# Optimization experiments

Measured on AMD Instinct MI355X. Metric: run time of the kernel, lower is better.

## Reference

```python
import jax, jax.numpy as jnp
import numpy as np

B, C, H, W = 4, 64, 96, 96
KS, NH = 7, 4


def setup_inputs() -> dict:
    key = jax.random.key(0)
    ks = jax.random.split(key, 9)
    s = 0.1  # keep logits in a sane range for softmax
    return {
        "input_x": jax.random.normal(ks[0], (B, C, H, W), jnp.float32),
        "q_w": jax.random.normal(ks[1], (C, C), jnp.float32) * s,
        "q_b": jax.random.normal(ks[2], (C,), jnp.float32) * s,
        "k_w": jax.random.normal(ks[3], (C, C), jnp.float32) * s,
        "k_b": jax.random.normal(ks[4], (C,), jnp.float32) * s,
        "v_w": jax.random.normal(ks[5], (C, C), jnp.float32) * s,
        "v_b": jax.random.normal(ks[6], (C,), jnp.float32) * s,
        "rel_h": jax.random.normal(ks[7], (C // 2, KS, 1), jnp.float32) * s,
        "rel_w": jax.random.normal(ks[8], (C // 2, 1, KS), jnp.float32) * s,
    }


def _unfold(x, ks):
    # x: (B, C, Hp, Wp) -> (B, C, Ho, Wo, ks, ks), same as torch .unfold(2).unfold(3)
    Hp, Wp = x.shape[2], x.shape[3]
    Ho, Wo = Hp - ks + 1, Wp - ks + 1
    ih = jnp.arange(Ho)[:, None] + jnp.arange(ks)[None, :]  # (Ho, ks)
    iw = jnp.arange(Wo)[:, None] + jnp.arange(ks)[None, :]  # (Wo, ks)
    return x[:, :, ih[:, None, :, None], iw[None, :, None, :]]


def reference(input_x, q_w, q_b, k_w, k_b, v_w, v_b, rel_h, rel_w):
    b, c, h, w = input_x.shape
    ks, nh = KS, NH
    dkh = c // nh
    p0 = (ks - 1) // 2
    p1 = ks - 1 - p0
    padded = jnp.pad(input_x, ((0, 0), (0, 0), (p0, p1), (p0, p1)))

    conv1x1 = lambda x, wt, bi: jnp.einsum('bchw,oc->bohw', x, wt) + bi[None, :, None, None]
    k = conv1x1(padded, k_w, k_b)
    v = conv1x1(padded, v_w, v_b)
    q = conv1x1(input_x, q_w, q_b)

    # flat reshapes exactly as in torch (row-major), reproducing its layout semantics
    k = _unfold(k, ks).reshape(b, nh, h, w, dkh, ks * ks)
    v = _unfold(v, ks).reshape(b, nh, h, w, dkh, ks * ks)
    q = q.reshape(b, nh, h, w, dkh)  # torch: (b,nh,h,w,dkh,1) squeezed

    qk = jnp.einsum('bnxyd,bnxydk->bnxyk', q, k).reshape(b, nh, h, w, ks, ks)
    # torch einsum 'bhxydz,cij->bhxyij' == (sum_d q) outer (sum_c rel)
    qsum = q.sum(-1)  # (b, nh, h, w)
    rel = rel_h.sum(0) + rel_w.sum(0)  # broadcasts to (ks, ks)
    qk = qk + qsum[..., None, None] * rel

    weights = jax.nn.softmax(qk.reshape(b, nh, h, w, ks * ks), axis=-1)
    attn = jnp.einsum('bnxyk,bnxydk->bnxyd', weights, v)  # (b, nh, h, w, dkh)
    attn = attn.reshape(b, c, h, w)  # flat reshape, matching torch
    return jax.nn.relu(attn)
```

## Files before the change

### kernel.cpp

```cpp
#include <hip/hip_runtime.h>

#define B_ 4
#define C_ 64
#define H_ 96
#define W_ 96
#define KS_ 7
#define NPIX (H_ * W_)
#define LDSTR 108

typedef __attribute__((ext_vector_type(8))) short short8;
typedef __attribute__((ext_vector_type(4))) float f32x4;

static __device__ inline ushort f2bf(float f) {
    union { float f; unsigned u; } v; v.f = f;
    unsigned r = (v.u + 0x7fff + ((v.u >> 16) & 1)) >> 16;
    return (ushort)r;
}


__global__ __launch_bounds__(256) void mfma_conv_kernel(
    const float* __restrict__ in,
    const float* __restrict__ qw, const float* __restrict__ qb,
    const float* __restrict__ kw, const float* __restrict__ kb,
    const float* __restrict__ vw, const float* __restrict__ vb,
    float* __restrict__ qkv)
{
    const int b    = blockIdx.y;
    const int pix0 = blockIdx.x * 32;
    const int t    = threadIdx.x;
    const int lane = t & 63;
    const int wv   = t >> 6;

    __shared__ ushort wlds[192 * 64];
    __shared__ ushort xs[32 * 64];
    __shared__ float  bias_s[192];

    #pragma unroll
    for (int g = 0; g < 12; ++g) {
        const int qq  = t + 256 * g;
        const int row = qq >> 4;
        const int c4  = (qq & 15) * 4;
        const float* src = (row < 64) ? qw + row * 64
                         : (row < 128) ? kw + (row - 64) * 64
                                       : vw + (row - 128) * 64;
        float4 f = *reinterpret_cast<const float4*>(src + c4);
        ushort4 u = make_ushort4(f2bf(f.x), f2bf(f.y), f2bf(f.z), f2bf(f.w));
        unsigned byte = (unsigned)(row * 128 + c4 * 2) ^ (unsigned)((row & 7) << 4);
        *reinterpret_cast<ushort4*>(reinterpret_cast<char*>(wlds) + byte) = u;
    }
    if (t < 192) {
        const int tensor = t >> 6;
        bias_s[t] = (tensor == 0 ? qb : tensor == 1 ? kb : vb)[t & 63];
    }
    {
        const int pix = t & 31, cg = t >> 5;
        const float* xp = in + (size_t)b * C_ * NPIX + pix0 + pix;
        #pragma unroll
        for (int g = 0; g < 2; ++g) {
            const int ch = (cg + 8 * g) * 4;
            float x0 = xp[(size_t)(ch    ) * NPIX];
            float x1 = xp[(size_t)(ch + 1) * NPIX];
            float x2 = xp[(size_t)(ch + 2) * NPIX];
            float x3 = xp[(size_t)(ch + 3) * NPIX];
            ushort4 u = make_ushort4(f2bf(x0), f2bf(x1), f2bf(x2), f2bf(x3));
            unsigned byte = (unsigned)(pix * 128 + ch * 2) ^ (unsigned)((pix & 7) << 4);
            *reinterpret_cast<ushort4*>(reinterpret_cast<char*>(xs) + byte) = u;
        }
    }
    __syncthreads();

    short8 afr[3][2];
    #pragma unroll
    for (int i = 0; i < 3; ++i) {
        const int row = (3 * wv + i) * 16 + (lane & 15);
        #pragma unroll
        for (int ka = 0; ka < 2; ++ka) {
            const int kk = ka * 32 + (lane >> 4) * 8;
            unsigned byte = (unsigned)(row * 128 + kk * 2) ^ (unsigned)((row & 7) << 4);
            afr[i][ka] = *reinterpret_cast<const short8*>(
                reinterpret_cast<const char*>(wlds) + byte);
        }
    }
    short8 bfr[2][2];
    #pragma unroll
    for (int nt = 0; nt < 2; ++nt) {
        const int pl = nt * 16 + (lane & 15);
        #pragma unroll
        for (int ka = 0; ka < 2; ++ka) {
            const int kk = ka * 32 + (lane >> 4) * 8;
            unsigned byte = (unsigned)(pl * 128 + kk * 2) ^ (unsigned)((pl & 7) << 4);
            bfr[nt][ka] = *reinterpret_cast<const short8*>(
                reinterpret_cast<const char*>(xs) + byte);
        }
    }
    f32x4 acc[3][2];
    #pragma unroll
    for (int i = 0; i < 3; ++i) {
        f32x4 bi;
        #pragma unroll
        for (int r = 0; r < 4; ++r)
            bi[r] = bias_s[(3 * wv + i) * 16 + (lane >> 4) * 4 + r];
        #pragma unroll
        for (int nt = 0; nt < 2; ++nt) acc[i][nt] = bi;
    }
    #pragma unroll
    for (int i = 0; i < 3; ++i) {
        #pragma unroll
        for (int nt = 0; nt < 2; ++nt) {
            acc[i][nt] = __builtin_amdgcn_mfma_f32_16x16x32_bf16(
                afr[i][0], bfr[nt][0], acc[i][nt], 0, 0, 0);
            acc[i][nt] = __builtin_amdgcn_mfma_f32_16x16x32_bf16(
                afr[i][1], bfr[nt][1], acc[i][nt], 0, 0, 0);
        }
    }
    #pragma unroll
    for (int i = 0; i < 3; ++i) {
        #pragma unroll
        for (int r = 0; r < 4; ++r) {
            const int row = (3 * wv + i) * 16 + (lane >> 4) * 4 + r;
            float* op = qkv + ((size_t)b * 192 + row) * NPIX + pix0 + (lane & 15);
            #pragma unroll
            for (int nt = 0; nt < 2; ++nt)
                op[nt * 16] = acc[i][nt][r];
        }
    }
}

__global__ __launch_bounds__(384) void attn_kernel(
    const float* __restrict__ qkv,
    const float* __restrict__ kb, const float* __restrict__ vb,
    const float* __restrict__ relh, const float* __restrict__ relw,
    float* __restrict__ out)
{
    const int bx   = blockIdx.x;
    const int tile = bx % 3;
    const int c    = (bx / 3) % C_;
    const int b    = bx / (3 * C_);
    const int ho0  = tile * 32;
    const int t    = threadIdx.x;

    __shared__ float ks[38 * LDSTR];
    __shared__ float vs[38 * LDSTR];
    __shared__ float rel_s[49];

    if (t < 49) {
        const int i = t / KS_, j = t % KS_;
        float s = 0.f;
        #pragma unroll
        for (int cc = 0; cc < C_ / 2; ++cc)
            s += relh[cc * KS_ + i] + relw[cc * KS_ + j];
        rel_s[t] = s;
    }
    {
        const float kbias = kb[c];
        const float vbias = vb[c];
        const float* kg = qkv + ((size_t)b * 192 +  64 + c) * NPIX;
        const float* vg = qkv + ((size_t)b * 192 + 128 + c) * NPIX;
        for (int idx = t; idx < 38 * 104; idx += 384) {
            const int rl = idx / 104, cl = idx - rl * 104;
            const int gr = ho0 + rl - 3, gc = cl - 3;
            const bool inb = (gr >= 0 && gr < H_ && gc >= 0 && gc < W_);
            const int gi = gr * W_ + gc;
            ks[rl * LDSTR + cl] = inb ? kg[gi] : kbias;
            vs[rl * LDSTR + cl] = inb ? vg[gi] : vbias;
        }
    }
    __syncthreads();

    const int r0   = t / 12;
    const int rest = t % 12;
    const int w0   = (rest >> 1) * 16;
    const int half = rest & 1;
    const int ho   = ho0 + r0;

    const float* qp = qkv + ((size_t)b * 192 + c) * NPIX + ho * W_ + w0;
    float qs[16];
    #pragma unroll
    for (int tt = 0; tt < 16; tt += 4) {
        float4 f = *reinterpret_cast<const float4*>(qp + tt);
        qs[tt] = f.x; qs[tt + 1] = f.y; qs[tt + 2] = f.z; qs[tt + 3] = f.w;
    }
    float qsum = 0.f;
    #pragma unroll
    for (int tt = 0; tt < 16; ++tt) qsum += qs[tt];

    float logit[49];
    #pragma unroll
    for (int i = 0; i < KS_; ++i) {
        float kr[22];
        const float* kp = &ks[(r0 + i) * LDSTR + w0];
        #pragma unroll
        for (int tt = 0; tt < 20; tt += 4) {
            float4 f = *reinterpret_cast<const float4*>(kp + tt);
            kr[tt] = f.x; kr[tt + 1] = f.y; kr[tt + 2] = f.z; kr[tt + 3] = f.w;
        }
        float2 f2 = *reinterpret_cast<const float2*>(kp + 20);
        kr[20] = f2.x; kr[21] = f2.y;
        #pragma unroll
        for (int j = 0; j < KS_; ++j) {
            float s0 = 0.f, s1 = 0.f, s2 = 0.f, s3 = 0.f;
            #pragma unroll
            for (int tt = 0; tt < 16; tt += 4) {
                s0 = fmaf(qs[tt],     kr[tt + j],     s0);
                s1 = fmaf(qs[tt + 1], kr[tt + 1 + j], s1);
                s2 = fmaf(qs[tt + 2], kr[tt + 2 + j], s2);
                s3 = fmaf(qs[tt + 3], kr[tt + 3 + j], s3);
            }
            logit[i * KS_ + j] = (s0 + s1) + (s2 + s3) + qsum * rel_s[i * KS_ + j];
        }
    }

    float m0 = logit[0], m1 = logit[1], m2 = logit[2], m3 = logit[3];
    #pragma unroll
    for (int kk = 4; kk < 48; kk += 4) {
        m0 = fmaxf(m0, logit[kk]);
        m1 = fmaxf(m1, logit[kk + 1]);
        m2 = fmaxf(m2, logit[kk + 2]);
        m3 = fmaxf(m3, logit[kk + 3]);
    }
    float m = fmaxf(fmaxf(m0, m1), fmaxf(m2, m3));
    m = fmaxf(m, logit[48]);

    float e0 = 0.f, e1 = 0.f, e2 = 0.f, e3 = 0.f;
    #pragma unroll
    for (int kk = 0; kk < 48; kk += 4) {
        float a0 = __expf(logit[kk]     - m);
        float a1 = __expf(logit[kk + 1] - m);
        float a2 = __expf(logit[kk + 2] - m);
        float a3 = __expf(logit[kk + 3] - m);
        logit[kk] = a0; logit[kk + 1] = a1; logit[kk + 2] = a2; logit[kk + 3] = a3;
        e0 += a0; e1 += a1; e2 += a2; e3 += a3;
    }
    float a48 = __expf(logit[48] - m);
    logit[48] = a48;
    const float inv = 1.f / ((e0 + e1) + (e2 + e3) + a48);

    float o8[8];
    #pragma unroll
    for (int d = 0; d < 8; ++d) o8[d] = 0.f;

    #pragma unroll
    for (int i = 0; i < KS_; ++i) {
        float vr[14];
        const float* vp = &vs[(r0 + i) * LDSTR + w0 + half * 8];
        #pragma unroll
        for (int tt = 0; tt < 12; tt += 4) {
            float4 f = *reinterpret_cast<const float4*>(vp + tt);
            vr[tt] = f.x; vr[tt + 1] = f.y; vr[tt + 2] = f.z; vr[tt + 3] = f.w;
        }
        float2 f2 = *reinterpret_cast<const float2*>(vp + 12);
        vr[12] = f2.x; vr[13] = f2.y;
        #pragma unroll
        for (int j = 0; j < KS_; ++j) {
            float wgt = logit[i * KS_ + j];
            #pragma unroll
            for (int d = 0; d < 8; ++d) o8[d] = fmaf(wgt, vr[d + j], o8[d]);
        }
    }

    float* op = out + (((size_t)b * C_ + c) * H_ + ho) * W_ + w0 + half * 8;
    #pragma unroll
    for (int d = 0; d < 8; d += 4) {
        float4 f;
        f.x = fmaxf(o8[d]     * inv, 0.f);
        f.y = fmaxf(o8[d + 1] * inv, 0.f);
        f.z = fmaxf(o8[d + 2] * inv, 0.f);
        f.w = fmaxf(o8[d + 3] * inv, 0.f);
        *reinterpret_cast<float4*>(op + d) = f;
    }
}

extern "C" void kernel_launch(void* const* d_in, const int* in_sizes, int n_in,
                              void* d_out, int out_size, void* d_ws, size_t ws_size,
                              hipStream_t stream) {
    const float* in   = (const float*)d_in[0];
    const float* qw   = (const float*)d_in[1];
    const float* qb   = (const float*)d_in[2];
    const float* kw   = (const float*)d_in[3];
    const float* kb   = (const float*)d_in[4];
    const float* vw   = (const float*)d_in[5];
    const float* vb   = (const float*)d_in[6];
    const float* relh = (const float*)d_in[7];
    const float* relw = (const float*)d_in[8];
    float* out = (float*)d_out;

    float* qkv = (float*)d_ws;

    dim3 cgrid(NPIX / 32, B_);
    mfma_conv_kernel<<<cgrid, 256, 0, stream>>>(in, qw, qb, kw, kb, vw, vb, qkv);

    dim3 agrid(B_ * C_ * 3);
    attn_kernel<<<agrid, 384, 0, stream>>>(qkv, kb, vb, relh, relw, out);
}
```

Before: 44.29 us.

## Load conv weights directly to registers, precompute rel table, store V as bf16

The conv kernel now reads weight fragments and biases straight from global memory into registers, removing the large LDS weight staging. It also computes the rel-position table once into workspace instead of having every attention block recompute it. The attention kernel loads the K/V halo four columns at a time, stores V in LDS as bf16 to halve its footprint, and switches the softmax to exp2 with log2e folded into q. These changes reduce LDS usage and redundant work, at the cost of bf16 rounding on V and uncoalesced weight reads.

Measured after the change: 42.70 us. 3.6% less time.

```diff
diff --git a/kernel.cpp b/kernel.cpp
--- a/kernel.cpp
+++ b/kernel.cpp
@@ -6,15 +6,20 @@
 #define W_ 96
 #define KS_ 7
 #define NPIX (H_ * W_)
-#define LDSTR 108
+#define LDK 108
+#define LDV 112
 
 typedef __attribute__((ext_vector_type(8))) short short8;
+typedef __attribute__((ext_vector_type(8))) unsigned short ushort8;
 typedef __attribute__((ext_vector_type(4))) float f32x4;
 
 static __device__ inline ushort f2bf(float f) {
     union { float f; unsigned u; } v; v.f = f;
     unsigned r = (v.u + 0x7fff + ((v.u >> 16) & 1)) >> 16;
     return (ushort)r;
+}
+static __device__ inline float bf2f(ushort u) {
+    union { unsigned u; float f; } v; v.u = ((unsigned)u) << 16; return v.f;
 }
 
 
@@ -23,7 +28,8 @@
     const float* __restrict__ qw, const float* __restrict__ qb,
     const float* __restrict__ kw, const float* __restrict__ kb,
     const float* __restrict__ vw, const float* __restrict__ vb,
-    float* __restrict__ qkv)
+    const float* __restrict__ relh, const float* __restrict__ relw,
+    float* __restrict__ qkv, float* __restrict__ rel_out)
 {
     const int b    = blockIdx.y;
     const int pix0 = blockIdx.x * 32;
@@ -31,27 +37,17 @@
     const int lane = t & 63;
     const int wv   = t >> 6;
 
-    __shared__ ushort wlds[192 * 64];
+    if (blockIdx.x == 0 && b == 0 && t < 49) {
+        const int i = t / KS_, j = t % KS_;
+        float s = 0.f;
+        #pragma unroll
+        for (int cc = 0; cc < C_ / 2; ++cc)
+            s += relh[cc * KS_ + i] + relw[cc * KS_ + j];
+        rel_out[t] = s;
+    }
+
     __shared__ ushort xs[32 * 64];
-    __shared__ float  bias_s[192];
-
-    #pragma unroll
-    for (int g = 0; g < 12; ++g) {
-        const int qq  = t + 256 * g;
-        const int row = qq >> 4;
-        const int c4  = (qq & 15) * 4;
-        const float* src = (row < 64) ? qw + row * 64
-                         : (row < 128) ? kw + (row - 64) * 64
-                                       : vw + (row - 128) * 64;
-        float4 f = *reinterpret_cast<const float4*>(src + c4);
-        ushort4 u = make_ushort4(f2bf(f.x), f2bf(f.y), f2bf(f.z), f2bf(f.w));
-        unsigned byte = (unsigned)(row * 128 + c4 * 2) ^ (unsigned)((row & 7) << 4);
-        *reinterpret_cast<ushort4*>(reinterpret_cast<char*>(wlds) + byte) = u;
-    }
-    if (t < 192) {
-        const int tensor = t >> 6;
-        bias_s[t] = (tensor == 0 ? qb : tensor == 1 ? kb : vb)[t & 63];
-    }
+
     {
         const int pix = t & 31, cg = t >> 5;
         const float* xp = in + (size_t)b * C_ * NPIX + pix0 + pix;
@@ -67,20 +63,37 @@
             *reinterpret_cast<ushort4*>(reinterpret_cast<char*>(xs) + byte) = u;
         }
     }
-    __syncthreads();
 
     short8 afr[3][2];
+    float  bi[3][4];
     #pragma unroll
     for (int i = 0; i < 3; ++i) {
-        const int row = (3 * wv + i) * 16 + (lane & 15);
+        const int mt  = 3 * wv + i;
+        const int row = mt * 16 + (lane & 15);
+        const float* wsrc = (mt < 4) ? qw + row * 64
+                          : (mt < 8) ? kw + (row - 64) * 64
+                                     : vw + (row - 128) * 64;
         #pragma unroll
         for (int ka = 0; ka < 2; ++ka) {
             const int kk = ka * 32 + (lane >> 4) * 8;
-            unsigned byte = (unsigned)(row * 128 + kk * 2) ^ (unsigned)((row & 7) << 4);
-            afr[i][ka] = *reinterpret_cast<const short8*>(
-                reinterpret_cast<const char*>(wlds) + byte);
-        }
-    }
+            float4 a = *reinterpret_cast<const float4*>(wsrc + kk);
+            float4 c = *reinterpret_cast<const float4*>(wsrc + kk + 4);
+            short8 s;
+            s[0] = (short)f2bf(a.x); s[1] = (short)f2bf(a.y);
+            s[2] = (short)f2bf(a.z); s[3] = (short)f2bf(a.w);
+            s[4] = (short)f2bf(c.x); s[5] = (short)f2bf(c.y);
+            s[6] = (short)f2bf(c.z); s[7] = (short)f2bf(c.w);
+            afr[i][ka] = s;
+        }
+        const int brow = mt * 16 + (lane >> 4) * 4;
+        const float* bsrc = (mt < 4) ? qb + brow
+                          : (mt < 8) ? kb + (brow - 64)
+                                     : vb + (brow - 128);
+        #pragma unroll
+        for (int r = 0; r < 4; ++r) bi[i][r] = bsrc[r];
+    }
+    __syncthreads();
+
     short8 bfr[2][2];
     #pragma unroll
     for (int nt = 0; nt < 2; ++nt) {
@@ -96,12 +109,11 @@
     f32x4 acc[3][2];
     #pragma unroll
     for (int i = 0; i < 3; ++i) {
-        f32x4 bi;
-        #pragma unroll
-        for (int r = 0; r < 4; ++r)
-            bi[r] = bias_s[(3 * wv + i) * 16 + (lane >> 4) * 4 + r];
-        #pragma unroll
-        for (int nt = 0; nt < 2; ++nt) acc[i][nt] = bi;
+        f32x4 bv;
+        #pragma unroll
+        for (int r = 0; r < 4; ++r) bv[r] = bi[i][r];
+        #pragma unroll
+        for (int nt = 0; nt < 2; ++nt) acc[i][nt] = bv;
     }
     #pragma unroll
     for (int i = 0; i < 3; ++i) {
@@ -129,8 +141,7 @@
 __global__ __launch_bounds__(384) void attn_kernel(
     const float* __restrict__ qkv,
     const float* __restrict__ kb, const float* __restrict__ vb,
-    const float* __restrict__ relh, const float* __restrict__ relw,
-    float* __restrict__ out)
+    const float* __restrict__ rel, float* __restrict__ out)
 {
     const int bx   = blockIdx.x;
     const int tile = bx % 3;
@@ -139,30 +150,37 @@
     const int ho0  = tile * 32;
     const int t    = threadIdx.x;
 
-    __shared__ float ks[38 * LDSTR];
-    __shared__ float vs[38 * LDSTR];
-    __shared__ float rel_s[49];
-
-    if (t < 49) {
-        const int i = t / KS_, j = t % KS_;
-        float s = 0.f;
-        #pragma unroll
-        for (int cc = 0; cc < C_ / 2; ++cc)
-            s += relh[cc * KS_ + i] + relw[cc * KS_ + j];
-        rel_s[t] = s;
-    }
-    {
-        const float kbias = kb[c];
-        const float vbias = vb[c];
-        const float* kg = qkv + ((size_t)b * 192 +  64 + c) * NPIX;
-        const float* vg = qkv + ((size_t)b * 192 + 128 + c) * NPIX;
-        for (int idx = t; idx < 38 * 104; idx += 384) {
-            const int rl = idx / 104, cl = idx - rl * 104;
-            const int gr = ho0 + rl - 3, gc = cl - 3;
-            const bool inb = (gr >= 0 && gr < H_ && gc >= 0 && gc < W_);
-            const int gi = gr * W_ + gc;
-            ks[rl * LDSTR + cl] = inb ? kg[gi] : kbias;
-            vs[rl * LDSTR + cl] = inb ? vg[gi] : vbias;
+    __shared__ float  ksl[38 * LDK];
+    __shared__ ushort vsl[38 * LDV];
+
+    const float kbias = kb[c];
+    const float vbias = vb[c];
+    const float* kg = qkv + ((size_t)b * 192 +  64 + c) * NPIX;
+    const float* vg = qkv + ((size_t)b * 192 + 128 + c) * NPIX;
+
+    #pragma unroll
+    for (int s0 = 0; s0 < 3; ++s0) {
+        const int slot = t + s0 * 384;
+        if (slot < 38 * 26) {
+            const int rl = slot / 26, c4 = (slot - rl * 26) * 4;
+            const int gr = ho0 + rl - 3;
+            const bool rin = (gr >= 0 && gr < H_);
+            const int grc = rin ? gr : 0;
+            float kv[4], vv[4];
+            #pragma unroll
+            for (int e = 0; e < 4; ++e) {
+                const int gc  = c4 + e - 3;
+                const bool inb = rin && (gc >= 0) && (gc < W_);
+                const int gcc = gc < 0 ? 0 : (gc > 95 ? 95 : gc);
+                const int gi  = grc * W_ + gcc;
+                const float kl = kg[gi], vl = vg[gi];
+                kv[e] = inb ? kl : kbias;
+                vv[e] = inb ? vl : vbias;
+            }
+            *reinterpret_cast<float4*>(&ksl[rl * LDK + c4]) =
+                make_float4(kv[0], kv[1], kv[2], kv[3]);
+            *reinterpret_cast<ushort4*>(&vsl[rl * LDV + c4]) =
+                make_ushort4(f2bf(vv[0]), f2bf(vv[1]), f2bf(vv[2]), f2bf(vv[3]));
         }
     }
     __syncthreads();
@@ -173,22 +191,24 @@
     const int half = rest & 1;
     const int ho   = ho0 + r0;
 
+    const float LOG2E = 1.44269504f;
     const float* qp = qkv + ((size_t)b * 192 + c) * NPIX + ho * W_ + w0;
     float qs[16];
     #pragma unroll
     for (int tt = 0; tt < 16; tt += 4) {
         float4 f = *reinterpret_cast<const float4*>(qp + tt);
-        qs[tt] = f.x; qs[tt + 1] = f.y; qs[tt + 2] = f.z; qs[tt + 3] = f.w;
+        qs[tt] = f.x * LOG2E; qs[tt + 1] = f.y * LOG2E;
+        qs[tt + 2] = f.z * LOG2E; qs[tt + 3] = f.w * LOG2E;
     }
     float qsum = 0.f;
     #pragma unroll
     for (int tt = 0; tt < 16; ++tt) qsum += qs[tt];
 
-    float logit[49];
+    float p[49];
     #pragma unroll
     for (int i = 0; i < KS_; ++i) {
         float kr[22];
-        const float* kp = &ks[(r0 + i) * LDSTR + w0];
+        const float* kp = &ksl[(r0 + i) * LDK + w0];
         #pragma unroll
         for (int tt = 0; tt < 20; tt += 4) {
             float4 f = *reinterpret_cast<const float4*>(kp + tt);
@@ -206,33 +226,30 @@
                 s2 = fmaf(qs[tt + 2], kr[tt + 2 + j], s2);
                 s3 = fmaf(qs[tt + 3], kr[tt + 3 + j], s3);
             }
-            logit[i * KS_ + j] = (s0 + s1) + (s2 + s3) + qsum * rel_s[i * KS_ + j];
-        }
-    }
-
-    float m0 = logit[0], m1 = logit[1], m2 = logit[2], m3 = logit[3];
+            p[i * KS_ + j] = (s0 + s1) + (s2 + s3) + qsum * rel[i * KS_ + j];
+        }
+    }
+
+    float m0 = p[0], m1 = p[1], m2 = p[2], m3 = p[3];
     #pragma unroll
     for (int kk = 4; kk < 48; kk += 4) {
-        m0 = fmaxf(m0, logit[kk]);
-        m1 = fmaxf(m1, logit[kk + 1]);
-        m2 = fmaxf(m2, logit[kk + 2]);
-        m3 = fmaxf(m3, logit[kk + 3]);
-    }
-    float m = fmaxf(fmaxf(m0, m1), fmaxf(m2, m3));
-    m = fmaxf(m, logit[48]);
+        m0 = fmaxf(m0, p[kk]);     m1 = fmaxf(m1, p[kk + 1]);
+        m2 = fmaxf(m2, p[kk + 2]); m3 = fmaxf(m3, p[kk + 3]);
+    }
+    float m = fmaxf(fmaxf(fmaxf(m0, m1), fmaxf(m2, m3)), p[48]);
 
     float e0 = 0.f, e1 = 0.f, e2 = 0.f, e3 = 0.f;
     #pragma unroll
     for (int kk = 0; kk < 48; kk += 4) {
-        float a0 = __expf(logit[kk]     - m);
-        float a1 = __expf(logit[kk + 1] - m);
-        float a2 = __expf(logit[kk + 2] - m);
-        float a3 = __expf(logit[kk + 3] - m);
-        logit[kk] = a0; logit[kk + 1] = a1; logit[kk + 2] = a2; logit[kk + 3] = a3;
+        float a0 = exp2f(p[kk]     - m);
+        float a1 = exp2f(p[kk + 1] - m);
+        float a2 = exp2f(p[kk + 2] - m);
+        float a3 = exp2f(p[kk + 3] - m);
+        p[kk] = a0; p[kk + 1] = a1; p[kk + 2] = a2; p[kk + 3] = a3;
         e0 += a0; e1 += a1; e2 += a2; e3 += a3;
     }
-    float a48 = __expf(logit[48] - m);
-    logit[48] = a48;
+    float a48 = exp2f(p[48] - m);
+    p[48] = a48;
     const float inv = 1.f / ((e0 + e1) + (e2 + e3) + a48);
 
     float o8[8];
@@ -241,20 +258,19 @@
 
     #pragma unroll
     for (int i = 0; i < KS_; ++i) {
-        float vr[14];
-        const float* vp = &vs[(r0 + i) * LDSTR + w0 + half * 8];
-        #pragma unroll
-        for (int tt = 0; tt < 12; tt += 4) {
-            float4 f = *reinterpret_cast<const float4*>(vp + tt);
-            vr[tt] = f.x; vr[tt + 1] = f.y; vr[tt + 2] = f.z; vr[tt + 3] = f.w;
-        }
-        float2 f2 = *reinterpret_cast<const float2*>(vp + 12);
-        vr[12] = f2.x; vr[13] = f2.y;
+        const ushort* vp = &vsl[(r0 + i) * LDV + w0 + half * 8];
+        ushort8 u0 = *reinterpret_cast<const ushort8*>(vp);
+        ushort8 u1 = *reinterpret_cast<const ushort8*>(vp + 8);
+        float vf[14];
+        #pragma unroll
+        for (int e = 0; e < 8; ++e) vf[e] = bf2f(u0[e]);
+        #pragma unroll
+        for (int e = 0; e < 6; ++e) vf[8 + e] = bf2f(u1[e]);
         #pragma unroll
         for (int j = 0; j < KS_; ++j) {
-            float wgt = logit[i * KS_ + j];
+            float wgt = p[i * KS_ + j];
             #pragma unroll
-            for (int d = 0; d < 8; ++d) o8[d] = fmaf(wgt, vr[d + j], o8[d]);
+            for (int d = 0; d < 8; ++d) o8[d] = fmaf(wgt, vf[d + j], o8[d]);
         }
     }
 
@@ -285,10 +301,12 @@
     float* out = (float*)d_out;
 
     float* qkv = (float*)d_ws;
+    float* rel = qkv + (size_t)B_ * 192 * NPIX;
 
     dim3 cgrid(NPIX / 32, B_);
-    mfma_conv_kernel<<<cgrid, 256, 0, stream>>>(in, qw, qb, kw, kb, vw, vb, qkv);
+    mfma_conv_kernel<<<cgrid, 256, 0, stream>>>(in, qw, qb, kw, kb, vw, vb,
+                                                relh, relw, qkv, rel);
 
     dim3 agrid(B_ * C_ * 3);
-    attn_kernel<<<agrid, 384, 0, stream>>>(qkv, kb, vb, relh, relw, out);
-}
+    attn_kernel<<<agrid, 384, 0, stream>>>(qkv, kb, vb, rel, out);
+}
```
